# Kernel tuning notes

Hardware: AMD Instinct MI355X
Metric: run time of the kernel (lower is better)

## Reference

```python
import jax, jax.numpy as jnp
import numpy as np
import math

B, H_IM, W_IM, HDIM, HEADS, PS = 16, 56, 56, 512, 8, 7


def setup_inputs() -> dict:
    key = jax.random.key(0)
    ks = jax.random.split(key, 4)
    x = jax.random.normal(ks[0], (B, H_IM * W_IM, HDIM), jnp.float32)
    mask = jnp.zeros((1, 1, H_IM, W_IM), jnp.bool_)
    Wqkv = jax.random.normal(ks[1], (HDIM, 3 * HDIM), jnp.float32) * 0.02
    Wproj = jax.random.normal(ks[2], (HDIM, HDIM), jnp.float32) * 0.02
    bproj = jnp.zeros((HDIM,), jnp.float32)
    rel_bias = jax.random.normal(ks[3], (HEADS, PS * PS, PS * PS), jnp.float32) * 0.02
    return {"x": x, "mask": mask, "Wqkv": Wqkv, "Wproj": Wproj,
            "bproj": bproj, "rel_bias": rel_bias, "H": H_IM, "W": W_IM}


def reference(x, mask, Wqkv, Wproj, bproj, rel_bias, H, W):
    b = x.shape[0]
    ps, g, hd = PS, HEADS, HDIM
    dh = hd // g
    scale = dh ** (-0.5)

    qkv = x @ Wqkv                                   # [b, H*W, 3*hd]
    qkv = qkv.reshape(b, H, W, 3 * hd)
    pad_b = int(math.ceil(H / ps)) * ps - H
    pad_r = int(math.ceil(W / ps)) * ps - W
    qkv = jnp.pad(qkv, ((0, 0), (0, pad_b), (0, pad_r), (0, 0)))
    kmask = jnp.pad(mask, ((0, 0), (0, 0), (0, pad_b), (0, pad_r)), constant_values=True)
    Hp, Wp = H + pad_b, W + pad_r
    sh, sw = Hp // ps, Wp // ps
    K, P = ps * ps, sh * sw

    # patchify: b (sh kh) (sw kw) c -> b (kh kw) (sh sw) c
    qkv = qkv.reshape(b, sh, ps, sw, ps, 3 * hd).transpose(0, 2, 4, 1, 3, 5).reshape(b, K, P, 3 * hd)
    kmask = kmask.reshape(1, 1, sh, ps, sw, ps).transpose(0, 1, 3, 5, 2, 4).reshape(1, 1, K, P)

    qkv = qkv.reshape(b, K, P, 3, g, dh)
    q, k, v = qkv[:, :, :, 0], qkv[:, :, :, 1], qkv[:, :, :, 2]  # each [b, K, P, g, dh]

    attn = jnp.einsum('bqpgc,bkpgc->bgqkp', q, k)    # [b, g, K, K, P]
    attn = (attn + rel_bias[None, :, :, :, None]) * scale
    m = kmask[:, None]                                # [1, 1, 1, K, P]
    attn = jnp.where(m, -jnp.inf, attn)
    attn = jax.nn.softmax(attn, axis=-2)              # softmax over key positions within window
    attn = jnp.where(m, 0.0, attn)

    out = jnp.einsum('bgqkp,bkpgc->bqpgc', attn, v)
    out = out.reshape(b, K, P, hd)
    # un-patchify: b (kh kw) (sh sw) c -> b (sh kh) (sw kw) c
    out = out.reshape(b, ps, ps, sh, sw, hd).transpose(0, 3, 1, 4, 2, 5).reshape(b, Hp, Wp, hd)
    out = out[:, :H, :W, :].reshape(b, H * W, hd)
    return out @ Wproj + bproj
```

## Files before the change

### kernel.cpp

```cpp
#include <hip/hip_runtime.h>
#include <hip/hip_bf16.h>

using bf16 = __hip_bfloat16;
using bf16x8 = __attribute__((ext_vector_type(8))) short;
using f32x4  = __attribute__((ext_vector_type(4))) float;

#define B_    16
#define HIM   56
#define WIM   56
#define HD    512
#define NHEAD 8
#define DH    64
#define NTOK  (HIM*WIM)
#define M_    (B_*NTOK)
#define K49   49

__device__ __forceinline__ void gload_lds16(const void* g, void* l) {
  __builtin_amdgcn_global_load_lds(
      (__attribute__((address_space(1))) const void*)g,
      (__attribute__((address_space(3))) void*)l, 16, 0, 0);
}

__global__ __launch_bounds__(256) void cvt_x_kernel(const float* __restrict__ in,
                                                    bf16* __restrict__ out) {
  size_t i = ((size_t)blockIdx.x * 256 + threadIdx.x) * 8;
  float4 a = *(const float4*)(in + i);
  float4 b = *(const float4*)(in + i + 4);
  union { uint4 v; bf16 h[8]; } o;
  o.h[0] = __float2bfloat16(a.x); o.h[1] = __float2bfloat16(a.y);
  o.h[2] = __float2bfloat16(a.z); o.h[3] = __float2bfloat16(a.w);
  o.h[4] = __float2bfloat16(b.x); o.h[5] = __float2bfloat16(b.y);
  o.h[6] = __float2bfloat16(b.z); o.h[7] = __float2bfloat16(b.w);
  *(uint4*)(out + i) = o.v;
}

__global__ __launch_bounds__(256) void cvt_transpose_kernel(const float* __restrict__ in,
                                                            bf16* __restrict__ out,
                                                            int K, int N) {
  int idx = blockIdx.x * 256 + threadIdx.x;
  int k = idx / N, n = idx - k * N;
  out[(size_t)n * K + k] = __float2bfloat16(in[idx]);
}

template<int N, bool OUT_BF16, bool BIAS>
__global__ __launch_bounds__(512, 2) void gemm256_kernel(
    const bf16* __restrict__ A,
    const bf16* __restrict__ Bt,
    void* __restrict__ Cp,
    const float* __restrict__ bias,
    int NBX)
{
  constexpr int K  = 512;
  constexpr int NK = K / 32;
  __shared__ alignas(16) bf16 lds[2][4][256 * 32];
  const int tid  = threadIdx.x;
  const int lane = tid & 63, wid = tid >> 6;
  const int l15  = lane & 15, kq = lane >> 4;
  const int wm   = wid >> 2,  wn = wid & 3;
  const int cpx = gridDim.x >> 3;
  const int wg  = (blockIdx.x & 7) * cpx + (blockIdx.x >> 3);
  const int by  = wg / NBX, bx = wg - by * NBX;
  const long arow0 = (long)by * 256;
  const long bcol0 = (long)bx * 256;

  auto stageHalf = [&](int ab, int j) {
    const bf16* g = (ab ? Bt + bcol0 * K : A + arow0 * K) + j * 32;
    bf16* lbase = &lds[ab][j & 3][0];
#pragma unroll
    for (int c = 0; c < 2; ++c) {
      int s   = c * 512 + tid;
      int row = s >> 2, sl = s & 3;
      int gs  = sl ^ ((row >> 1) & 3);
      gload_lds16((const char*)(g + (long)row * K) + gs * 16,
                  lbase + (c * 512 + wid * 64) * 8);
    }
  };

  f32x4 acc[8][4] = {};

#define KSLICE(SL, VMSTR, DOSTAGE, JSTAGE) {                                            \
    asm volatile("s_waitcnt vmcnt(" VMSTR ")" ::: "memory");                            \
    __builtin_amdgcn_s_barrier();                                                       \
    bf16x8 af[8], bb[4];                                                                \
    _Pragma("unroll")                                                                   \
    for (int mt = 0; mt < 8; ++mt) {                                                    \
      int row = wm * 128 + mt * 16 + l15;                                               \
      af[mt] = *(const bf16x8*)&lds[0][SL][row * 32 + ((kq ^ ((row >> 1) & 3)) << 3)];  \
    }                                                                                   \
    _Pragma("unroll")                                                                   \
    for (int nt = 0; nt < 4; ++nt) {                                                    \
      int row = wn * 64 + nt * 16 + l15;                                                \
      bb[nt] = *(const bf16x8*)&lds[1][SL][row * 32 + ((kq ^ ((row >> 1) & 3)) << 3)];  \
    }                                                                                   \
    if (DOSTAGE) { stageHalf(0, JSTAGE); stageHalf(1, JSTAGE); }                        \
    __builtin_amdgcn_s_setprio(1);                                                      \
    _Pragma("unroll")                                                                   \
    for (int mt = 0; mt < 8; ++mt)                                                      \
      _Pragma("unroll")                                                                 \
      for (int nt = 0; nt < 4; ++nt)                                                    \
        acc[mt][nt] = __builtin_amdgcn_mfma_f32_16x16x32_bf16(bb[nt], af[mt],           \
                                                              acc[mt][nt], 0, 0, 0);    \
    __builtin_amdgcn_s_setprio(0);                                                      \
  }

  stageHalf(0, 0); stageHalf(1, 0);
  stageHalf(0, 1); stageHalf(1, 1);
  stageHalf(0, 2); stageHalf(1, 2);

#pragma unroll 1
  for (int jo = 0; jo < NK - 4; jo += 4) {
    KSLICE(0, "8", true, jo + 3);
    KSLICE(1, "8", true, jo + 4);
    KSLICE(2, "8", true, jo + 5);
    KSLICE(3, "8", true, jo + 6);
  }
  KSLICE(0, "8", true,  15);
  KSLICE(1, "8", false, 0);
  KSLICE(2, "4", false, 0);
  KSLICE(3, "0", false, 0);
#undef KSLICE

  const long crow0 = arow0 + wm * 128;
  const long ccol0 = bcol0 + wn * 64 + kq * 4;
#pragma unroll
  for (int mt = 0; mt < 8; ++mt) {
    long row = crow0 + mt * 16 + l15;
#pragma unroll
    for (int nt = 0; nt < 4; ++nt) {
      long col = ccol0 + nt * 16;
      if (OUT_BF16) {
        union { unsigned long long u; unsigned short h[4]; } pk;
#pragma unroll
        for (int r = 0; r < 4; ++r) {
          bf16 hh = __float2bfloat16(acc[mt][nt][r]);
          pk.h[r] = *(unsigned short*)&hh;
        }
        __builtin_nontemporal_store(pk.u,
            (unsigned long long*)((bf16*)Cp + row * N + col));
      } else {
        f32x4 o = acc[mt][nt];
        if (BIAS) {
          o[0] += bias[col];     o[1] += bias[col + 1];
          o[2] += bias[col + 2]; o[3] += bias[col + 3];
        }
        __builtin_nontemporal_store(o, (f32x4*)((float*)Cp + row * N + col));
      }
    }
  }
}

__global__ __launch_bounds__(256) void attn_win_kernel(
    const bf16* __restrict__ qkv, const float* __restrict__ rb, bf16* __restrict__ outa)
{
  __shared__ alignas(16) bf16 Qs[64 * 72];
  __shared__ alignas(16) bf16 Ks[64 * 72];
  __shared__ alignas(16) bf16 Vt[64 * 72];
  __shared__ alignas(16) bf16 Ps[64 * 72];
  const int tid = threadIdx.x, lane = tid & 63, wid = tid >> 6;
  const int p = blockIdx.x, g = blockIdx.y, b = blockIdx.z;
  const int sh = p >> 3, sw = p & 7;
  const size_t nb = (size_t)b * NTOK;
  const int c8 = (tid & 7) * 8;

#pragma unroll
  for (int it = 0; it < 2; ++it) {
    int t = (tid >> 3) + it * 32;
    uint4 vq = {0, 0, 0, 0}, vk = vq, vv = vq;
    if (t < K49) {
      int ph = t / 7, pw = t - ph * 7;
      int n = (sh * 7 + ph) * WIM + sw * 7 + pw;
      const bf16* src = qkv + (nb + n) * 1536 + g * 64 + c8;
      vq = *(const uint4*)(src);
      vk = *(const uint4*)(src + 512);
      vv = *(const uint4*)(src + 1024);
    }
    *(uint4*)&Qs[t * 72 + c8] = vq;
    *(uint4*)&Ks[t * 72 + c8] = vk;
    union { uint4 u; unsigned short s[8]; } uv; uv.u = vv;
    unsigned short* vt16 = (unsigned short*)Vt;
#pragma unroll
    for (int e = 0; e < 8; ++e) vt16[(c8 + e) * 72 + t] = uv.s[e];
  }
  __syncthreads();

  const int l15 = lane & 15, kq = lane >> 4;
  bf16x8 aq[2];
#pragma unroll
  for (int kk = 0; kk < 2; ++kk)
    aq[kk] = *(const bf16x8*)&Qs[(wid * 16 + l15) * 72 + kk * 32 + kq * 8];
  float sv[4][4];
#pragma unroll
  for (int ct = 0; ct < 4; ++ct) {
    f32x4 acc = {0.f, 0.f, 0.f, 0.f};
#pragma unroll
    for (int kk = 0; kk < 2; ++kk) {
      bf16x8 bk = *(const bf16x8*)&Ks[(ct * 16 + l15) * 72 + kk * 32 + kq * 8];
      acc = __builtin_amdgcn_mfma_f32_16x16x32_bf16(aq[kk], bk, acc, 0, 0, 0);
    }
    int kcol = ct * 16 + l15;
#pragma unroll
    for (int r = 0; r < 4; ++r) {
      int q = wid * 16 + kq * 4 + r;
      float bias = (q < K49 && kcol < K49) ? rb[((size_t)g * K49 + q) * K49 + kcol] : 0.f;
      float v = (acc[r] + bias) * 0.125f;
      sv[ct][r] = (kcol < K49) ? v : -1e30f;
    }
  }
#pragma unroll
  for (int r = 0; r < 4; ++r) {
    float m = fmaxf(fmaxf(sv[0][r], sv[1][r]), fmaxf(sv[2][r], sv[3][r]));
#pragma unroll
    for (int d = 1; d < 16; d <<= 1) m = fmaxf(m, __shfl_xor(m, d));
    float e0 = __expf(sv[0][r] - m), e1 = __expf(sv[1][r] - m);
    float e2 = __expf(sv[2][r] - m), e3 = __expf(sv[3][r] - m);
    float s = e0 + e1 + e2 + e3;
#pragma unroll
    for (int d = 1; d < 16; d <<= 1) s += __shfl_xor(s, d);
    float inv = 1.0f / s;
    int q = wid * 16 + kq * 4 + r;
    Ps[q * 72 +  0 + l15] = __float2bfloat16(e0 * inv);
    Ps[q * 72 + 16 + l15] = __float2bfloat16(e1 * inv);
    Ps[q * 72 + 32 + l15] = __float2bfloat16(e2 * inv);
    Ps[q * 72 + 48 + l15] = __float2bfloat16(e3 * inv);
  }
  __syncthreads();
  bf16x8 ap[2];
#pragma unroll
  for (int kk = 0; kk < 2; ++kk)
    ap[kk] = *(const bf16x8*)&Ps[(wid * 16 + l15) * 72 + kk * 32 + kq * 8];
#pragma unroll
  for (int ct = 0; ct < 4; ++ct) {
    f32x4 acc = {0.f, 0.f, 0.f, 0.f};
#pragma unroll
    for (int kk = 0; kk < 2; ++kk) {
      bf16x8 bv = *(const bf16x8*)&Vt[(ct * 16 + l15) * 72 + kk * 32 + kq * 8];
      acc = __builtin_amdgcn_mfma_f32_16x16x32_bf16(ap[kk], bv, acc, 0, 0, 0);
    }
#pragma unroll
    for (int r = 0; r < 4; ++r) {
      int q = wid * 16 + kq * 4 + r;
      if (q < K49) {
        int ph = q / 7, pw = q - ph * 7;
        int n = (sh * 7 + ph) * WIM + sw * 7 + pw;
        outa[(nb + n) * HD + g * 64 + ct * 16 + l15] = __float2bfloat16(acc[r]);
      }
    }
  }
}

extern "C" void kernel_launch(void* const* d_in, const int* in_sizes, int n_in,
                              void* d_out, int out_size, void* d_ws, size_t ws_size,
                              hipStream_t stream) {
  (void)in_sizes; (void)n_in; (void)out_size;
  const float* x     = (const float*)d_in[0];
  const float* wqkv  = (const float*)d_in[2];
  const float* wproj = (const float*)d_in[3];
  const float* bproj = (const float*)d_in[4];
  const float* rb    = (const float*)d_in[5];

  char* ws = (char*)d_ws;
  bf16* x_bf    = (bf16*)(ws);
  bf16* wqkv_t  = (bf16*)(ws + 51380224);
  bf16* wproj_t = (bf16*)(ws + 52953088);
  bf16* qkv     = (bf16*)(ws + 53477376);
  bf16* attno   = x_bf;
  float* out    = (float*)d_out;
  if (ws_size < 207618048) return;

  cvt_x_kernel<<<dim3(12544), 256, 0, stream>>>(x, x_bf);
  cvt_transpose_kernel<<<dim3(3072), 256, 0, stream>>>(wqkv, wqkv_t, 512, 1536);
  cvt_transpose_kernel<<<dim3(1024), 256, 0, stream>>>(wproj, wproj_t, 512, 512);
  gemm256_kernel<1536, true, false><<<dim3(1176), 512, 0, stream>>>(
      x_bf, wqkv_t, (void*)qkv, nullptr, 6);
  attn_win_kernel<<<dim3(64, NHEAD, B_), 256, 0, stream>>>(qkv, rb, attno);
  gemm256_kernel<512, false, true><<<dim3(392), 512, 0, stream>>>(
      attno, wproj_t, (void*)out, bproj, 2);
}
```

Before: 256.4 us.

## Use 1024-thread GEMM blocks and process all heads per window in one block

The GEMM kernel now runs 16 waves per 256x256 tile instead of 8. Each wave owns a 64x64 sub-tile with fewer accumulators, and each thread issues one async LDS load per stage. The aim is more waves to hide latency and lower register pressure. The windowed attention kernel now handles all 8 heads of a window in one 512-thread block, with one wave per head, whole-row coalesced Q/K/V loads, and a shared LDS buffer reused for Q, K and P. Risks are larger LDS use and occupancy limits under the 1024-thread launch bounds, plus extra barriers and a skewed V transpose.

```diff
diff --git a/kernel.cpp b/kernel.cpp
--- a/kernel.cpp
+++ b/kernel.cpp
@@ -43,7 +43,7 @@
 }
 
 template<int N, bool OUT_BF16, bool BIAS>
-__global__ __launch_bounds__(512, 2) void gemm256_kernel(
+__global__ __launch_bounds__(1024, 4) void gemm256b_kernel(
     const bf16* __restrict__ A,
     const bf16* __restrict__ Bt,
     void* __restrict__ Cp,
@@ -65,41 +65,34 @@
 
   auto stageHalf = [&](int ab, int j) {
     const bf16* g = (ab ? Bt + bcol0 * K : A + arow0 * K) + j * 32;
-    bf16* lbase = &lds[ab][j & 3][0];
-#pragma unroll
-    for (int c = 0; c < 2; ++c) {
-      int s   = c * 512 + tid;
-      int row = s >> 2, sl = s & 3;
-      int gs  = sl ^ ((row >> 1) & 3);
-      gload_lds16((const char*)(g + (long)row * K) + gs * 16,
-                  lbase + (c * 512 + wid * 64) * 8);
-    }
+    int row = tid >> 2, sl = tid & 3;
+    int gs  = sl ^ ((row >> 1) & 3);
+    gload_lds16((const char*)(g + (long)row * K) + gs * 16,
+                &lds[ab][j & 3][wid * 64 * 8]);
   };
 
-  f32x4 acc[8][4] = {};
+  f32x4 acc[4][4] = {};
 
 #define KSLICE(SL, VMSTR, DOSTAGE, JSTAGE) {                                            \
     asm volatile("s_waitcnt vmcnt(" VMSTR ")" ::: "memory");                            \
     __builtin_amdgcn_s_barrier();                                                       \
-    bf16x8 af[8], bb[4];                                                                \
-    _Pragma("unroll")                                                                   \
-    for (int mt = 0; mt < 8; ++mt) {                                                    \
-      int row = wm * 128 + mt * 16 + l15;                                               \
-      af[mt] = *(const bf16x8*)&lds[0][SL][row * 32 + ((kq ^ ((row >> 1) & 3)) << 3)];  \
-    }                                                                                   \
+    if (DOSTAGE) { stageHalf(0, JSTAGE); stageHalf(1, JSTAGE); }                        \
+    bf16x8 bb[4];                                                                       \
     _Pragma("unroll")                                                                   \
     for (int nt = 0; nt < 4; ++nt) {                                                    \
       int row = wn * 64 + nt * 16 + l15;                                                \
       bb[nt] = *(const bf16x8*)&lds[1][SL][row * 32 + ((kq ^ ((row >> 1) & 3)) << 3)];  \
     }                                                                                   \
-    if (DOSTAGE) { stageHalf(0, JSTAGE); stageHalf(1, JSTAGE); }                        \
     __builtin_amdgcn_s_setprio(1);                                                      \
     _Pragma("unroll")                                                                   \
-    for (int mt = 0; mt < 8; ++mt)                                                      \
+    for (int mt = 0; mt < 4; ++mt) {                                                    \
+      int row = wm * 64 + mt * 16 + l15;                                                \
+      bf16x8 af = *(const bf16x8*)&lds[0][SL][row * 32 + ((kq ^ ((row >> 1) & 3)) << 3)];\
       _Pragma("unroll")                                                                 \
       for (int nt = 0; nt < 4; ++nt)                                                    \
-        acc[mt][nt] = __builtin_amdgcn_mfma_f32_16x16x32_bf16(bb[nt], af[mt],           \
+        acc[mt][nt] = __builtin_amdgcn_mfma_f32_16x16x32_bf16(bb[nt], af,               \
                                                               acc[mt][nt], 0, 0, 0);    \
+    }                                                                                   \
     __builtin_amdgcn_s_setprio(0);                                                      \
   }
 
@@ -109,21 +102,21 @@
 
 #pragma unroll 1
   for (int jo = 0; jo < NK - 4; jo += 4) {
-    KSLICE(0, "8", true, jo + 3);
-    KSLICE(1, "8", true, jo + 4);
-    KSLICE(2, "8", true, jo + 5);
-    KSLICE(3, "8", true, jo + 6);
-  }
-  KSLICE(0, "8", true,  15);
-  KSLICE(1, "8", false, 0);
-  KSLICE(2, "4", false, 0);
+    KSLICE(0, "4", true, jo + 3);
+    KSLICE(1, "4", true, jo + 4);
+    KSLICE(2, "4", true, jo + 5);
+    KSLICE(3, "4", true, jo + 6);
+  }
+  KSLICE(0, "4", true,  15);
+  KSLICE(1, "4", false, 0);
+  KSLICE(2, "2", false, 0);
   KSLICE(3, "0", false, 0);
 #undef KSLICE
 
-  const long crow0 = arow0 + wm * 128;
+  const long crow0 = arow0 + wm * 64;
   const long ccol0 = bcol0 + wn * 64 + kq * 4;
 #pragma unroll
-  for (int mt = 0; mt < 8; ++mt) {
+  for (int mt = 0; mt < 4; ++mt) {
     long row = crow0 + mt * 16 + l15;
 #pragma unroll
     for (int nt = 0; nt < 4; ++nt) {
@@ -149,103 +142,143 @@
   }
 }
 
-__global__ __launch_bounds__(256) void attn_win_kernel(
+__global__ __launch_bounds__(512) void attn_win2_kernel(
     const bf16* __restrict__ qkv, const float* __restrict__ rb, bf16* __restrict__ outa)
 {
-  __shared__ alignas(16) bf16 Qs[64 * 72];
-  __shared__ alignas(16) bf16 Ks[64 * 72];
-  __shared__ alignas(16) bf16 Vt[64 * 72];
-  __shared__ alignas(16) bf16 Ps[64 * 72];
+  __shared__ alignas(16) bf16 KsR[64 * 528];
+  __shared__ alignas(16) bf16 Vt[512 * 72];
   const int tid = threadIdx.x, lane = tid & 63, wid = tid >> 6;
-  const int p = blockIdx.x, g = blockIdx.y, b = blockIdx.z;
+  const int p = blockIdx.x, b = blockIdx.y;
   const int sh = p >> 3, sw = p & 7;
   const size_t nb = (size_t)b * NTOK;
-  const int c8 = (tid & 7) * 8;
-
-#pragma unroll
-  for (int it = 0; it < 2; ++it) {
-    int t = (tid >> 3) + it * 32;
-    uint4 vq = {0, 0, 0, 0}, vk = vq, vv = vq;
+  const int l15 = lane & 15, kq = lane >> 4;
+  const int g = wid;
+
+  auto nOf = [&](int t) { int ph = t / 7, pw = t - ph * 7;
+                          return (sh * 7 + ph) * WIM + sw * 7 + pw; };
+
+  unsigned short* vt16 = (unsigned short*)Vt;
+#pragma unroll
+  for (int it = 0; it < 8; ++it) {
+    int t = it * 8 + wid;
+    int ch = lane * 8;
+    uint4 vq = {0, 0, 0, 0}, vv = vq;
     if (t < K49) {
-      int ph = t / 7, pw = t - ph * 7;
-      int n = (sh * 7 + ph) * WIM + sw * 7 + pw;
-      const bf16* src = qkv + (nb + n) * 1536 + g * 64 + c8;
+      const bf16* src = qkv + (nb + nOf(t)) * 1536 + ch;
       vq = *(const uint4*)(src);
-      vk = *(const uint4*)(src + 512);
       vv = *(const uint4*)(src + 1024);
     }
-    *(uint4*)&Qs[t * 72 + c8] = vq;
-    *(uint4*)&Ks[t * 72 + c8] = vk;
+    *(uint4*)&KsR[t * 528 + ch] = vq;
     union { uint4 u; unsigned short s[8]; } uv; uv.u = vv;
-    unsigned short* vt16 = (unsigned short*)Vt;
-#pragma unroll
-    for (int e = 0; e < 8; ++e) vt16[(c8 + e) * 72 + t] = uv.s[e];
+#pragma unroll
+    for (int i = 0; i < 8; ++i) {
+      int e = (i + lane) & 7;
+      vt16[(ch + e) * 72 + t] = uv.s[e];
+    }
   }
   __syncthreads();
 
-  const int l15 = lane & 15, kq = lane >> 4;
-  bf16x8 aq[2];
-#pragma unroll
-  for (int kk = 0; kk < 2; ++kk)
-    aq[kk] = *(const bf16x8*)&Qs[(wid * 16 + l15) * 72 + kk * 32 + kq * 8];
-  float sv[4][4];
-#pragma unroll
-  for (int ct = 0; ct < 4; ++ct) {
-    f32x4 acc = {0.f, 0.f, 0.f, 0.f};
-#pragma unroll
-    for (int kk = 0; kk < 2; ++kk) {
-      bf16x8 bk = *(const bf16x8*)&Ks[(ct * 16 + l15) * 72 + kk * 32 + kq * 8];
-      acc = __builtin_amdgcn_mfma_f32_16x16x32_bf16(aq[kk], bk, acc, 0, 0, 0);
-    }
-    int kcol = ct * 16 + l15;
+  bf16x8 aq[4][2];
+#pragma unroll
+  for (int mt = 0; mt < 4; ++mt)
+#pragma unroll
+    for (int kk = 0; kk < 2; ++kk)
+      aq[mt][kk] = *(const bf16x8*)&KsR[(mt * 16 + l15) * 528 + g * 64 + kk * 32 + kq * 8];
+  __syncthreads();
+
+#pragma unroll
+  for (int it = 0; it < 8; ++it) {
+    int t = it * 8 + wid;
+    int ch = lane * 8;
+    uint4 vk = {0, 0, 0, 0};
+    if (t < K49) vk = *(const uint4*)(qkv + (nb + nOf(t)) * 1536 + 512 + ch);
+    *(uint4*)&KsR[t * 528 + ch] = vk;
+  }
+  __syncthreads();
+
+  bf16x8 bk[4][2];
+#pragma unroll
+  for (int ct = 0; ct < 4; ++ct)
+#pragma unroll
+    for (int kk = 0; kk < 2; ++kk)
+      bk[ct][kk] = *(const bf16x8*)&KsR[(ct * 16 + l15) * 528 + g * 64 + kk * 32 + kq * 8];
+  f32x4 accS[4][4] = {};
+#pragma unroll
+  for (int mt = 0; mt < 4; ++mt)
+#pragma unroll
+    for (int ct = 0; ct < 4; ++ct)
+#pragma unroll
+      for (int kk = 0; kk < 2; ++kk)
+        accS[mt][ct] = __builtin_amdgcn_mfma_f32_16x16x32_bf16(aq[mt][kk], bk[ct][kk],
+                                                               accS[mt][ct], 0, 0, 0);
+#pragma unroll
+  for (int mt = 0; mt < 4; ++mt)
+#pragma unroll
+    for (int ct = 0; ct < 4; ++ct) {
+      int kcol = ct * 16 + l15;
+#pragma unroll
+      for (int r = 0; r < 4; ++r) {
+        int q = mt * 16 + kq * 4 + r;
+        float x = accS[mt][ct][r];
+        if (q < K49 && kcol < K49) x += rb[((size_t)g * K49 + q) * K49 + kcol];
+        x *= 0.125f;
+        accS[mt][ct][r] = (kcol < K49) ? x : -1e30f;
+      }
+    }
+#pragma unroll
+  for (int mt = 0; mt < 4; ++mt)
 #pragma unroll
     for (int r = 0; r < 4; ++r) {
-      int q = wid * 16 + kq * 4 + r;
-      float bias = (q < K49 && kcol < K49) ? rb[((size_t)g * K49 + q) * K49 + kcol] : 0.f;
-      float v = (acc[r] + bias) * 0.125f;
-      sv[ct][r] = (kcol < K49) ? v : -1e30f;
-    }
-  }
-#pragma unroll
-  for (int r = 0; r < 4; ++r) {
-    float m = fmaxf(fmaxf(sv[0][r], sv[1][r]), fmaxf(sv[2][r], sv[3][r]));
-#pragma unroll
-    for (int d = 1; d < 16; d <<= 1) m = fmaxf(m, __shfl_xor(m, d));
-    float e0 = __expf(sv[0][r] - m), e1 = __expf(sv[1][r] - m);
-    float e2 = __expf(sv[2][r] - m), e3 = __expf(sv[3][r] - m);
-    float s = e0 + e1 + e2 + e3;
-#pragma unroll
-    for (int d = 1; d < 16; d <<= 1) s += __shfl_xor(s, d);
-    float inv = 1.0f / s;
-    int q = wid * 16 + kq * 4 + r;
-    Ps[q * 72 +  0 + l15] = __float2bfloat16(e0 * inv);
-    Ps[q * 72 + 16 + l15] = __float2bfloat16(e1 * inv);
-    Ps[q * 72 + 32 + l15] = __float2bfloat16(e2 * inv);
-    Ps[q * 72 + 48 + l15] = __float2bfloat16(e3 * inv);
-  }
-  __syncthreads();
-  bf16x8 ap[2];
-#pragma unroll
-  for (int kk = 0; kk < 2; ++kk)
-    ap[kk] = *(const bf16x8*)&Ps[(wid * 16 + l15) * 72 + kk * 32 + kq * 8];
-#pragma unroll
-  for (int ct = 0; ct < 4; ++ct) {
-    f32x4 acc = {0.f, 0.f, 0.f, 0.f};
-#pragma unroll
-    for (int kk = 0; kk < 2; ++kk) {
-      bf16x8 bv = *(const bf16x8*)&Vt[(ct * 16 + l15) * 72 + kk * 32 + kq * 8];
-      acc = __builtin_amdgcn_mfma_f32_16x16x32_bf16(ap[kk], bv, acc, 0, 0, 0);
-    }
+      float m = fmaxf(fmaxf(accS[mt][0][r], accS[mt][1][r]),
+                      fmaxf(accS[mt][2][r], accS[mt][3][r]));
+#pragma unroll
+      for (int d = 1; d < 16; d <<= 1) m = fmaxf(m, __shfl_xor(m, d));
+      float e0 = __expf(accS[mt][0][r] - m), e1 = __expf(accS[mt][1][r] - m);
+      float e2 = __expf(accS[mt][2][r] - m), e3 = __expf(accS[mt][3][r] - m);
+      float s = e0 + e1 + e2 + e3;
+#pragma unroll
+      for (int d = 1; d < 16; d <<= 1) s += __shfl_xor(s, d);
+      float inv = 1.0f / s;
+      int q = mt * 16 + kq * 4 + r;
+      bf16* pd = &KsR[q * 528 + g * 64 + l15];
+      pd[ 0] = __float2bfloat16(e0 * inv);
+      pd[16] = __float2bfloat16(e1 * inv);
+      pd[32] = __float2bfloat16(e2 * inv);
+      pd[48] = __float2bfloat16(e3 * inv);
+    }
+
+  bf16x8 ap[4][2], bv[4][2];
+#pragma unroll
+  for (int mt = 0; mt < 4; ++mt)
+#pragma unroll
+    for (int kk = 0; kk < 2; ++kk)
+      ap[mt][kk] = *(const bf16x8*)&KsR[(mt * 16 + l15) * 528 + g * 64 + kk * 32 + kq * 8];
+#pragma unroll
+  for (int ct = 0; ct < 4; ++ct)
+#pragma unroll
+    for (int kk = 0; kk < 2; ++kk)
+      bv[ct][kk] = *(const bf16x8*)&Vt[(g * 64 + ct * 16 + l15) * 72 + kk * 32 + kq * 8];
+  f32x4 accO[4][4] = {};
+#pragma unroll
+  for (int mt = 0; mt < 4; ++mt)
+#pragma unroll
+    for (int ct = 0; ct < 4; ++ct)
+#pragma unroll
+      for (int kk = 0; kk < 2; ++kk)
+        accO[mt][ct] = __builtin_amdgcn_mfma_f32_16x16x32_bf16(ap[mt][kk], bv[ct][kk],
+                                                               accO[mt][ct], 0, 0, 0);
+#pragma unroll
+  for (int mt = 0; mt < 4; ++mt)
 #pragma unroll
     for (int r = 0; r < 4; ++r) {
-      int q = wid * 16 + kq * 4 + r;
+      int q = mt * 16 + kq * 4 + r;
       if (q < K49) {
-        int ph = q / 7, pw = q - ph * 7;
-        int n = (sh * 7 + ph) * WIM + sw * 7 + pw;
-        outa[(nb + n) * HD + g * 64 + ct * 16 + l15] = __float2bfloat16(acc[r]);
+        bf16* dst = outa + (nb + nOf(q)) * HD + g * 64 + l15;
+#pragma unroll
+        for (int ct = 0; ct < 4; ++ct)
+          dst[ct * 16] = __float2bfloat16(accO[mt][ct][r]);
       }
     }
-  }
 }
 
 extern "C" void kernel_launch(void* const* d_in, const int* in_sizes, int n_in,
@@ -270,9 +303,9 @@
   cvt_x_kernel<<<dim3(12544), 256, 0, stream>>>(x, x_bf);
   cvt_transpose_kernel<<<dim3(3072), 256, 0, stream>>>(wqkv, wqkv_t, 512, 1536);
   cvt_transpose_kernel<<<dim3(1024), 256, 0, stream>>>(wproj, wproj_t, 512, 512);
-  gemm256_kernel<1536, true, false><<<dim3(1176), 512, 0, stream>>>(
+  gemm256b_kernel<1536, true, false><<<dim3(1176), 1024, 0, stream>>>(
       x_bf, wqkv_t, (void*)qkv, nullptr, 6);
-  attn_win_kernel<<<dim3(64, NHEAD, B_), 256, 0, stream>>>(qkv, rb, attno);
-  gemm256_kernel<512, false, true><<<dim3(392), 512, 0, stream>>>(
+  attn_win2_kernel<<<dim3(64, B_), 512, 0, stream>>>(qkv, rb, attno);
+  gemm256b_kernel<512, false, true><<<dim3(392), 1024, 0, stream>>>(
       attno, wproj_t, (void*)out, bproj, 2);
 }
```

After: 291.4 us. 13.7% more time.
